# Performance work log

Measured on AMD Instinct MI355X. Metric: run time of the kernel, lower is better.

The kernel has to match this reference:

```python
import jax, jax.numpy as jnp
import numpy as np
from jax import lax

B = 65536
IMG = 28
K = 3
OUT_HW = IMG - K + 1  # 26
FLAT = OUT_HW * OUT_HW  # 676
HID = 100
NCLS = 10


def setup_inputs() -> dict:
    key = jax.random.key(0)
    ks = jax.random.split(key, 6)
    x = jax.random.normal(ks[0], (B, IMG * IMG), dtype=jnp.float32)
    conv_w = jax.random.normal(ks[1], (K, K), dtype=jnp.float32)
    # Linear params, PyTorch layout: weight [out, in], bias [out]
    w1 = jax.random.normal(ks[2], (HID, FLAT), dtype=jnp.float32) * (1.0 / np.sqrt(FLAT))
    b1 = jax.random.normal(ks[3], (HID,), dtype=jnp.float32) * 0.01
    w2 = jax.random.normal(ks[4], (NCLS, HID), dtype=jnp.float32) * (1.0 / np.sqrt(HID))
    b2 = jax.random.normal(ks[5], (NCLS,), dtype=jnp.float32) * 0.01
    return {"x": x, "conv_w": conv_w, "w1": w1, "b1": b1, "w2": w2, "b2": b2}


def reference(x, conv_w, w1, b1, w2, b2):
    # x: [B, 784] -> [B, 1, 28, 28]
    img = x.reshape(-1, 1, IMG, IMG)
    # Cross-correlation (matches the slice*weight sum in Convolve), valid padding
    kern = conv_w[None, None, :, :]  # [O=1, I=1, 3, 3]
    conv = lax.conv_general_dilated(
        img, kern, window_strides=(1, 1), padding="VALID",
        dimension_numbers=("NCHW", "OIHW", "NCHW"),
    )  # [B, 1, 26, 26]
    feat = conv.reshape(conv.shape[0], FLAT)
    h1 = jax.nn.relu(feat @ w1.T + b1)
    return h1 @ w2.T + b2  # [B, 10]
```

## Files before the change

kernel.cpp:

```cpp
#include <hip/hip_runtime.h>

#define IMG 28
#define FLATK 784
#define OHW 26
#define FLAT 676
#define HID 100
#define NCLS 10
#define KP 800
#define BM 256
#define BSTRIDE 808

typedef __attribute__((ext_vector_type(8))) short bfrag;
typedef __attribute__((ext_vector_type(4))) float f32x4;
typedef __attribute__((ext_vector_type(4))) unsigned int u32x4;

__device__ __forceinline__ unsigned short f2bf(float f) {
    unsigned u = __float_as_uint(f);
    u = (u + 0x7fffu + ((u >> 16) & 1u)) >> 16;
    return (unsigned short)u;
}

__global__ void build_weights(const float* __restrict__ conv_w,
                              const float* __restrict__ w1,
                              const float* __restrict__ w2,
                              unsigned short* __restrict__ w1b,
                              unsigned short* __restrict__ w2b) {
    int idx = blockIdx.x * blockDim.x + threadIdx.x;
    if (idx < 128 * KP) {
        int n = idx / KP, k = idx - n * KP;
        float val = 0.f;
        if (n < HID && k < FLATK) {
            int qr = k / IMG, qc = k % IMG;
            #pragma unroll
            for (int i = 0; i < 3; ++i) {
                int r = qr - i;
                if (r < 0 || r >= OHW) continue;
                #pragma unroll
                for (int j = 0; j < 3; ++j) {
                    int c = qc - j;
                    if (c < 0 || c >= OHW) continue;
                    val += conv_w[i * 3 + j] * w1[n * FLAT + r * OHW + c];
                }
            }
        }
        w1b[idx] = f2bf(val);
    } else {
        int t = idx - 128 * KP;
        if (t < 16 * 128) {
            int n = t >> 7, k = t & 127;
            float v = (n < NCLS && k < HID) ? w2[n * HID + k] : 0.f;
            w2b[t] = f2bf(v);
        }
    }
}

#define LOADA(PH, S) do {                                                      \
    int k_ = (S) * 32 + (khi << 3);                                            \
    if (k_ >= FLATK) k_ -= FLATK;     \
    pre[PH][0] = *(const f32x4*)(xr0 + k_);                                    \
    pre[PH][1] = *(const f32x4*)(xr0 + k_ + 4);                                \
    pre[PH][2] = *(const f32x4*)(xr1 + k_);                                    \
    pre[PH][3] = *(const f32x4*)(xr1 + k_ + 4);                                \
} while (0)

#define COMP(PH, S) do {                                                       \
    union { u32x4 u; bfrag b; } a0_, a1_;                                      \
    asm("v_cvt_pk_bf16_f32 %0, %1, %2" : "=v"(a0_.u.x) : "v"(pre[PH][0].x), "v"(pre[PH][0].y)); \
    asm("v_cvt_pk_bf16_f32 %0, %1, %2" : "=v"(a0_.u.y) : "v"(pre[PH][0].z), "v"(pre[PH][0].w)); \
    asm("v_cvt_pk_bf16_f32 %0, %1, %2" : "=v"(a0_.u.z) : "v"(pre[PH][1].x), "v"(pre[PH][1].y)); \
    asm("v_cvt_pk_bf16_f32 %0, %1, %2" : "=v"(a0_.u.w) : "v"(pre[PH][1].z), "v"(pre[PH][1].w)); \
    asm("v_cvt_pk_bf16_f32 %0, %1, %2" : "=v"(a1_.u.x) : "v"(pre[PH][2].x), "v"(pre[PH][2].y)); \
    asm("v_cvt_pk_bf16_f32 %0, %1, %2" : "=v"(a1_.u.y) : "v"(pre[PH][2].z), "v"(pre[PH][2].w)); \
    asm("v_cvt_pk_bf16_f32 %0, %1, %2" : "=v"(a1_.u.z) : "v"(pre[PH][3].x), "v"(pre[PH][3].y)); \
    asm("v_cvt_pk_bf16_f32 %0, %1, %2" : "=v"(a1_.u.w) : "v"(pre[PH][3].z), "v"(pre[PH][3].w)); \
    _Pragma("unroll")                                                          \
    for (int nt = 0; nt < 7; ++nt) {                                           \
        int n_ = (nt < 6) ? ((nt << 4) + r15) : (84 + r15);                    \
        const bfrag bw = *(const bfrag*)(Blds + (size_t)n_ * BSTRIDE           \
                                         + (S) * 32 + (khi << 3));             \
        acc0[nt] = __builtin_amdgcn_mfma_f32_16x16x32_bf16(a0_.b, bw, acc0[nt], 0, 0, 0); \
        acc1[nt] = __builtin_amdgcn_mfma_f32_16x16x32_bf16(a1_.b, bw, acc1[nt], 0, 0, 0); \
    }                                                                          \
} while (0)

__global__ __launch_bounds__(512) void fused_fwd(
    const float* __restrict__ x,
    const unsigned short* __restrict__ w1b,
    const float* __restrict__ b1,
    const unsigned short* __restrict__ w2b,
    const float* __restrict__ b2,
    float* __restrict__ out)
{
    __shared__ char smem[100 * BSTRIDE * 2] __attribute__((aligned(128)));
    unsigned short* Blds = (unsigned short*)smem;

    const int tid  = threadIdx.x;
    const int lane = tid & 63;
    const int wv   = tid >> 6;
    const int r15  = lane & 15;
    const int khi  = lane >> 4;
    const int row0 = blockIdx.x * BM;

    for (int i = tid; i < 100 * 100; i += 512) {
        int n = i / 100, kv = i - n * 100;
        *(bfrag*)(Blds + (size_t)n * BSTRIDE + (kv << 3)) =
            *(const bfrag*)(w1b + (size_t)n * KP + (kv << 3));
    }
    __syncthreads();

    const float* xr0 = x + (size_t)(row0 + (wv << 5) + r15) * FLATK;
    const float* xr1 = xr0 + 16 * FLATK;

    f32x4 acc0[7], acc1[7];
    #pragma unroll
    for (int n = 0; n < 7; ++n) {
        acc0[n] = f32x4{0.f, 0.f, 0.f, 0.f};
        acc1[n] = f32x4{0.f, 0.f, 0.f, 0.f};
    }

    f32x4 pre[3][4];

    LOADA(0, 0); LOADA(1, 1); LOADA(2, 2);

    COMP(0, 0);  LOADA(0, 3);   COMP(1, 1);  LOADA(1, 4);   COMP(2, 2);  LOADA(2, 5);
    COMP(0, 3);  LOADA(0, 6);   COMP(1, 4);  LOADA(1, 7);   COMP(2, 5);  LOADA(2, 8);
    COMP(0, 6);  LOADA(0, 9);   COMP(1, 7);  LOADA(1, 10);  COMP(2, 8);  LOADA(2, 11);
    COMP(0, 9);  LOADA(0, 12);  COMP(1, 10); LOADA(1, 13);  COMP(2, 11); LOADA(2, 14);
    COMP(0, 12); LOADA(0, 15);  COMP(1, 13); LOADA(1, 16);  COMP(2, 14); LOADA(2, 17);
    COMP(0, 15); LOADA(0, 18);  COMP(1, 16); LOADA(1, 19);  COMP(2, 17); LOADA(2, 20);
    COMP(0, 18); LOADA(0, 21);  COMP(1, 19); LOADA(1, 22);  COMP(2, 20); LOADA(2, 23);
    COMP(0, 21); LOADA(0, 24);  COMP(1, 22);                COMP(2, 23);
    COMP(0, 24);

    __syncthreads();

    unsigned short (*H1)[136] = (unsigned short (*)[136])smem;
    for (int i = tid; i < 256 * 28; i += 512) {
        int r = i / 28, c = 100 + (i - (i / 28) * 28);
        H1[r][c] = 0;
    }
    #pragma unroll
    for (int nt = 0; nt < 7; ++nt) {
        int col = (nt < 6) ? ((nt << 4) + r15) : (84 + r15);
        bool wr = (nt < 6) || (col >= 96);
        float bias = (col < HID) ? b1[col] : 0.f;
        int rb0 = (wv << 5) + (khi << 2);
        if (wr) {
            #pragma unroll
            for (int q = 0; q < 4; ++q) {
                float v0 = acc0[nt][q] + bias;
                float v1 = acc1[nt][q] + bias;
                H1[rb0 + q][col]      = f2bf(fmaxf(v0, 0.f));
                H1[rb0 + 16 + q][col] = f2bf(fmaxf(v1, 0.f));
            }
        }
    }
    __syncthreads();

    f32x4 acc2[2] = {f32x4{0.f,0.f,0.f,0.f}, f32x4{0.f,0.f,0.f,0.f}};
    #pragma unroll
    for (int ks = 0; ks < 4; ++ks) {
        const bfrag bwv = *(const bfrag*)(w2b + r15 * 128 + (ks << 5) + (khi << 3));
        #pragma unroll
        for (int mf = 0; mf < 2; ++mf) {
            int r = (wv << 5) + (mf << 4) + r15;
            const bfrag ah = *(const bfrag*)&H1[r][(ks << 5) + (khi << 3)];
            acc2[mf] = __builtin_amdgcn_mfma_f32_16x16x32_bf16(ah, bwv, acc2[mf], 0, 0, 0);
        }
    }

    if (r15 < NCLS) {
        float bias2 = b2[r15];
        #pragma unroll
        for (int mf = 0; mf < 2; ++mf) {
            int rbase = row0 + (wv << 5) + (mf << 4) + (khi << 2);
            #pragma unroll
            for (int q = 0; q < 4; ++q)
                out[(size_t)(rbase + q) * NCLS + r15] = acc2[mf][q] + bias2;
        }
    }
}

extern "C" void kernel_launch(void* const* d_in, const int* in_sizes, int n_in,
                              void* d_out, int out_size, void* d_ws, size_t ws_size,
                              hipStream_t stream) {
    const float* x      = (const float*)d_in[0];
    const float* conv_w = (const float*)d_in[1];
    const float* w1     = (const float*)d_in[2];
    const float* b1     = (const float*)d_in[3];
    const float* w2     = (const float*)d_in[4];
    const float* b2     = (const float*)d_in[5];
    float* out = (float*)d_out;

    unsigned short* w1b = (unsigned short*)d_ws;
    unsigned short* w2b = w1b + 128 * KP;

    build_weights<<<(128 * KP + 16 * 128 + 255) / 256, 256, 0, stream>>>(conv_w, w1, w2, w1b, w2b);
    fused_fwd<<<65536 / BM, 512, 0, stream>>>(x, w1b, b1, w2b, b2, out);
}
```

Baseline: 48.15 us.

## Remap K-dimension so each lane reads contiguous 200-element chunk of input row

Changes the K-index permutation for the MFMA inner product: each of the four lane groups now owns a contiguous 200-element span of the row (kq = khi*200), not interleaved 8-element slices. Each lane loads 16 contiguous floats per phase and feeds two MFMA steps, with double buffering in place of triple buffering. The aim is longer contiguous per-lane global reads and fewer, larger load batches. The trade-off is a different per-wave coalescing pattern and wrap handling on each of the four sub-loads.

New measurement: 94.17 us. 95.6% more time.

```diff
diff --git a/kernel.cpp b/kernel.cpp
--- a/kernel.cpp
+++ b/kernel.cpp
@@ -54,30 +54,38 @@
     }
 }
 
-#define LOADA(PH, S) do {                                                      \
-    int k_ = (S) * 32 + (khi << 3);                                            \
-    if (k_ >= FLATK) k_ -= FLATK;     \
-    pre[PH][0] = *(const f32x4*)(xr0 + k_);                                    \
-    pre[PH][1] = *(const f32x4*)(xr0 + k_ + 4);                                \
-    pre[PH][2] = *(const f32x4*)(xr1 + k_);                                    \
-    pre[PH][3] = *(const f32x4*)(xr1 + k_ + 4);                                \
+
+#define LOADP(PH, T) do {                                                      \
+    int a0 = kq + (T) * 16, a1 = a0 + 4, a2 = a0 + 8, a3 = a0 + 12;            \
+    if (a0 >= FLATK) a0 -= FLATK;                                              \
+    if (a1 >= FLATK) a1 -= FLATK;                                              \
+    if (a2 >= FLATK) a2 -= FLATK;                                              \
+    if (a3 >= FLATK) a3 -= FLATK;                                              \
+    pre[PH][0] = *(const f32x4*)(xr0 + a0);                                    \
+    pre[PH][1] = *(const f32x4*)(xr0 + a1);                                    \
+    pre[PH][2] = *(const f32x4*)(xr0 + a2);                                    \
+    pre[PH][3] = *(const f32x4*)(xr0 + a3);                                    \
+    pre[PH][4] = *(const f32x4*)(xr1 + a0);                                    \
+    pre[PH][5] = *(const f32x4*)(xr1 + a1);                                    \
+    pre[PH][6] = *(const f32x4*)(xr1 + a2);                                    \
+    pre[PH][7] = *(const f32x4*)(xr1 + a3);                                    \
 } while (0)
 
-#define COMP(PH, S) do {                                                       \
+#define COMPH(PH, H, S) do {                                                   \
     union { u32x4 u; bfrag b; } a0_, a1_;                                      \
-    asm("v_cvt_pk_bf16_f32 %0, %1, %2" : "=v"(a0_.u.x) : "v"(pre[PH][0].x), "v"(pre[PH][0].y)); \
-    asm("v_cvt_pk_bf16_f32 %0, %1, %2" : "=v"(a0_.u.y) : "v"(pre[PH][0].z), "v"(pre[PH][0].w)); \
-    asm("v_cvt_pk_bf16_f32 %0, %1, %2" : "=v"(a0_.u.z) : "v"(pre[PH][1].x), "v"(pre[PH][1].y)); \
-    asm("v_cvt_pk_bf16_f32 %0, %1, %2" : "=v"(a0_.u.w) : "v"(pre[PH][1].z), "v"(pre[PH][1].w)); \
-    asm("v_cvt_pk_bf16_f32 %0, %1, %2" : "=v"(a1_.u.x) : "v"(pre[PH][2].x), "v"(pre[PH][2].y)); \
-    asm("v_cvt_pk_bf16_f32 %0, %1, %2" : "=v"(a1_.u.y) : "v"(pre[PH][2].z), "v"(pre[PH][2].w)); \
-    asm("v_cvt_pk_bf16_f32 %0, %1, %2" : "=v"(a1_.u.z) : "v"(pre[PH][3].x), "v"(pre[PH][3].y)); \
-    asm("v_cvt_pk_bf16_f32 %0, %1, %2" : "=v"(a1_.u.w) : "v"(pre[PH][3].z), "v"(pre[PH][3].w)); \
+    asm("v_cvt_pk_bf16_f32 %0, %1, %2" : "=v"(a0_.u.x) : "v"(pre[PH][(H)*2].x),   "v"(pre[PH][(H)*2].y)); \
+    asm("v_cvt_pk_bf16_f32 %0, %1, %2" : "=v"(a0_.u.y) : "v"(pre[PH][(H)*2].z),   "v"(pre[PH][(H)*2].w)); \
+    asm("v_cvt_pk_bf16_f32 %0, %1, %2" : "=v"(a0_.u.z) : "v"(pre[PH][(H)*2+1].x), "v"(pre[PH][(H)*2+1].y)); \
+    asm("v_cvt_pk_bf16_f32 %0, %1, %2" : "=v"(a0_.u.w) : "v"(pre[PH][(H)*2+1].z), "v"(pre[PH][(H)*2+1].w)); \
+    asm("v_cvt_pk_bf16_f32 %0, %1, %2" : "=v"(a1_.u.x) : "v"(pre[PH][(H)*2+4].x), "v"(pre[PH][(H)*2+4].y)); \
+    asm("v_cvt_pk_bf16_f32 %0, %1, %2" : "=v"(a1_.u.y) : "v"(pre[PH][(H)*2+4].z), "v"(pre[PH][(H)*2+4].w)); \
+    asm("v_cvt_pk_bf16_f32 %0, %1, %2" : "=v"(a1_.u.z) : "v"(pre[PH][(H)*2+5].x), "v"(pre[PH][(H)*2+5].y)); \
+    asm("v_cvt_pk_bf16_f32 %0, %1, %2" : "=v"(a1_.u.w) : "v"(pre[PH][(H)*2+5].z), "v"(pre[PH][(H)*2+5].w)); \
     _Pragma("unroll")                                                          \
     for (int nt = 0; nt < 7; ++nt) {                                           \
         int n_ = (nt < 6) ? ((nt << 4) + r15) : (84 + r15);                    \
         const bfrag bw = *(const bfrag*)(Blds + (size_t)n_ * BSTRIDE           \
-                                         + (S) * 32 + (khi << 3));             \
+                                         + kq + (S) * 8);                      \
         acc0[nt] = __builtin_amdgcn_mfma_f32_16x16x32_bf16(a0_.b, bw, acc0[nt], 0, 0, 0); \
         acc1[nt] = __builtin_amdgcn_mfma_f32_16x16x32_bf16(a1_.b, bw, acc1[nt], 0, 0, 0); \
     }                                                                          \
@@ -99,6 +107,7 @@
     const int wv   = tid >> 6;
     const int r15  = lane & 15;
     const int khi  = lane >> 4;
+    const int kq   = khi * 200;
     const int row0 = blockIdx.x * BM;
 
     for (int i = tid; i < 100 * 100; i += 512) {
@@ -118,19 +127,23 @@
         acc1[n] = f32x4{0.f, 0.f, 0.f, 0.f};
     }
 
-    f32x4 pre[3][4];
-
-    LOADA(0, 0); LOADA(1, 1); LOADA(2, 2);
-
-    COMP(0, 0);  LOADA(0, 3);   COMP(1, 1);  LOADA(1, 4);   COMP(2, 2);  LOADA(2, 5);
-    COMP(0, 3);  LOADA(0, 6);   COMP(1, 4);  LOADA(1, 7);   COMP(2, 5);  LOADA(2, 8);
-    COMP(0, 6);  LOADA(0, 9);   COMP(1, 7);  LOADA(1, 10);  COMP(2, 8);  LOADA(2, 11);
-    COMP(0, 9);  LOADA(0, 12);  COMP(1, 10); LOADA(1, 13);  COMP(2, 11); LOADA(2, 14);
-    COMP(0, 12); LOADA(0, 15);  COMP(1, 13); LOADA(1, 16);  COMP(2, 14); LOADA(2, 17);
-    COMP(0, 15); LOADA(0, 18);  COMP(1, 16); LOADA(1, 19);  COMP(2, 17); LOADA(2, 20);
-    COMP(0, 18); LOADA(0, 21);  COMP(1, 19); LOADA(1, 22);  COMP(2, 20); LOADA(2, 23);
-    COMP(0, 21); LOADA(0, 24);  COMP(1, 22);                COMP(2, 23);
-    COMP(0, 24);
+    f32x4 pre[2][8];
+
+    LOADP(0, 0); LOADP(1, 1);
+
+    COMPH(0, 0, 0);  COMPH(0, 1, 1);  LOADP(0, 2);
+    COMPH(1, 0, 2);  COMPH(1, 1, 3);  LOADP(1, 3);
+    COMPH(0, 0, 4);  COMPH(0, 1, 5);  LOADP(0, 4);
+    COMPH(1, 0, 6);  COMPH(1, 1, 7);  LOADP(1, 5);
+    COMPH(0, 0, 8);  COMPH(0, 1, 9);  LOADP(0, 6);
+    COMPH(1, 0, 10); COMPH(1, 1, 11); LOADP(1, 7);
+    COMPH(0, 0, 12); COMPH(0, 1, 13); LOADP(0, 8);
+    COMPH(1, 0, 14); COMPH(1, 1, 15); LOADP(1, 9);
+    COMPH(0, 0, 16); COMPH(0, 1, 17); LOADP(0, 10);
+    COMPH(1, 0, 18); COMPH(1, 1, 19); LOADP(1, 11);
+    COMPH(0, 0, 20); COMPH(0, 1, 21); LOADP(0, 12);
+    COMPH(1, 0, 22); COMPH(1, 1, 23);
+    COMPH(0, 0, 24);
 
     __syncthreads();
 
```
